# Performance work log

Hardware: AMD Instinct MI355X
Metric: run time of the kernel (lower is better)

The kernel has to match this reference:

```python
import jax, jax.numpy as jnp
import numpy as np

WSCALE = 0.05  # keep ReLU MLP activations in a sane range


def setup_inputs() -> dict:
    key = jax.random.key(0)
    ks = jax.random.split(key, 9)
    B, D, H = 2048, 64, 512
    return {
        "x": jax.random.normal(ks[0], (B, D), dtype=jnp.float32),
        "W1": jax.random.normal(ks[1], (H, D), dtype=jnp.float32) * WSCALE,
        "b1": jax.random.normal(ks[2], (H,), dtype=jnp.float32) * WSCALE,
        "W2": jax.random.normal(ks[3], (H, H), dtype=jnp.float32) * WSCALE,
        "b2": jax.random.normal(ks[4], (H,), dtype=jnp.float32) * WSCALE,
        "W3": jax.random.normal(ks[5], (H, H), dtype=jnp.float32) * WSCALE,
        "b3": jax.random.normal(ks[6], (H,), dtype=jnp.float32) * WSCALE,
        "W4": jax.random.normal(ks[7], (D, H), dtype=jnp.float32) * WSCALE,
        "b4": jax.random.normal(ks[8], (D,), dtype=jnp.float32) * WSCALE,
    }


def reference(x, W1, b1, W2, b2, W3, b3, W4, b4):
    # Score network: ReLU MLP (weights stored PyTorch-style [out, in]).
    a1 = x @ W1.T + b1          # [B, H]
    h1 = jax.nn.relu(a1)
    a2 = h1 @ W2.T + b2
    h2 = jax.nn.relu(a2)
    a3 = h2 @ W3.T + b3
    h3 = jax.nn.relu(a3)
    s = h3 @ W4.T + b4          # [B, D] score

    # Divergence = trace of Jacobian ds/dx per sample.
    # Per-sample J = W4 @ diag(m3) @ W3 @ diag(m2) @ W2 @ diag(m1) @ W1,
    # with m_k = 1[a_k > 0] (ReLU derivative; 0 at 0 like torch autograd).
    m1 = (a1 > 0).astype(x.dtype)
    m2 = (a2 > 0).astype(x.dtype)
    m3 = (a3 > 0).astype(x.dtype)
    T = m1[:, :, None] * W1[None, :, :]                 # [B, H, D]
    T = m2[:, :, None] * jnp.einsum('ij,bjd->bid', W2, T)  # [B, H, D]
    T = m3[:, :, None] * jnp.einsum('ij,bjd->bid', W3, T)  # [B, H, D]
    div = jnp.einsum('dj,bjd->b', W4, T)                # trace of J, [B]

    # Hyvarinen score: 0.5 * ||s||^2 + div
    val = 0.5 * jnp.sum(s * s, axis=1) + div
    return val
```

## Files before the change

kernel.cpp:

```cpp
#include <hip/hip_runtime.h>
#include <stdint.h>


typedef __attribute__((ext_vector_type(8))) short short8;
typedef __attribute__((ext_vector_type(4))) float f32x4;

union U16x8 {
  uint4 u;
  short8 s;
};

__device__ __forceinline__ uint16_t f2bf(float f) {
  uint32_t u = __float_as_uint(f);
  uint32_t lsb = (u >> 16) & 1u;
  u += 0x7FFFu + lsb;
  return (uint16_t)(u >> 16);
}

__device__ __forceinline__ void lds_load16(const uint4* gsrc, uint4* ldst) {
  __builtin_amdgcn_global_load_lds(
      (const __attribute__((address_space(1))) void*)gsrc,
      (__attribute__((address_space(3))) void*)ldst, 16, 0, 0);
}

__global__ __launch_bounds__(256) void convert_kernel(
    const float* __restrict__ W1, const float* __restrict__ W2,
    const float* __restrict__ W3, const float* __restrict__ W4,
    uint16_t* __restrict__ A2swz, uint16_t* __restrict__ A3swz,
    uint16_t* __restrict__ B1swz, uint16_t* __restrict__ B4swz,
    float* __restrict__ W2Tf, float* __restrict__ W3Tf,
    float* __restrict__ W1Tf, float* __restrict__ W4Tf) {
  const int i = blockIdx.x * 256 + threadIdx.x;
  if (i < 262144) {
    const int e = i;
    const int f = e >> 3, j = e & 7;
    const int lane = f & 63, fk = f >> 6;
    const int kc = fk & 15, r16 = fk >> 4;
    const int l15 = lane & 15, quad = lane >> 4;
    const int row = r16 * 16 + l15, col = kc * 32 + quad * 8 + j;
    A2swz[e] = f2bf(W2[row * 512 + col]);
  } else if (i < 524288) {
    const int e = i - 262144;
    const int f = e >> 3, j = e & 7;
    const int lane = f & 63, fk = f >> 6;
    const int kc = fk & 15, r16 = fk >> 4;
    const int l15 = lane & 15, quad = lane >> 4;
    const int row = r16 * 16 + l15, col = kc * 32 + quad * 8 + j;
    A3swz[e] = f2bf(W3[col * 512 + row]);
  } else if (i < 557056) {
    const int e = i - 524288;
    const int f = e >> 3, j = e & 7;
    const int lane = f & 63, fk = f >> 6;
    const int kc = fk >> 2, jt = fk & 3;
    const int l15 = lane & 15, quad = lane >> 4;
    const int d = jt * 16 + l15, col = kc * 32 + quad * 8 + j;
    B1swz[e] = f2bf(W1[col * 64 + d]);
  } else if (i < 589824) {
    const int e = i - 557056;
    const int f = e >> 3, j = e & 7;
    const int lane = f & 63, fk = f >> 6;
    const int kc = fk >> 2, jt = fk & 3;
    const int l15 = lane & 15, quad = lane >> 4;
    const int d = jt * 16 + l15, col = kc * 32 + quad * 8 + j;
    B4swz[e] = f2bf(W4[d * 512 + col]);
  } else if (i < 851968) {
    const int e = i - 589824;
    const int k = e >> 9, jj = e & 511;
    W2Tf[e] = W2[jj * 512 + k];
  } else if (i < 1114112) {
    const int e = i - 851968;
    const int k = e >> 9, jj = e & 511;
    W3Tf[e] = W3[jj * 512 + k];
  } else if (i < 1146880) {
    const int e = i - 1114112;
    const int k = e >> 9, jj = e & 511;
    W1Tf[e] = W1[jj * 64 + k];
  } else if (i < 1179648) {
    const int e = i - 1146880;
    const int k = e >> 6, d = e & 63;
    W4Tf[e] = W4[d * 512 + k];
  }
}

__device__ __forceinline__ void relu_store_mask4(
    float acc[4], float (*hdst)[4], uint32_t* __restrict__ mbase,
    int t, int lane, int wv) {
#pragma unroll
  for (int s = 0; s < 4; ++s) {
    const unsigned long long bal = __ballot(acc[s] > 0.f);
    if (lane == 0) {
      uint2 w2;
      w2.x = (uint32_t)bal;
      w2.y = (uint32_t)(bal >> 32);
      *(uint2*)(mbase + (size_t)s * 16 + 2 * wv) = w2;
    }
  }
  float4 r;
  r.x = acc[0] > 0.f ? acc[0] : 0.f;
  r.y = acc[1] > 0.f ? acc[1] : 0.f;
  r.z = acc[2] > 0.f ? acc[2] : 0.f;
  r.w = acc[3] > 0.f ? acc[3] : 0.f;
  *(float4*)&hdst[t][0] = r;
}

__global__ __launch_bounds__(512) void forward_kernel(
    const float* __restrict__ x,
    const float* __restrict__ W1Tf, const float* __restrict__ b1,
    const float* __restrict__ W2Tf, const float* __restrict__ b2,
    const float* __restrict__ W3Tf, const float* __restrict__ b3,
    const float* __restrict__ W4Tf, const float* __restrict__ b4,
    uint32_t* __restrict__ m1p, uint32_t* __restrict__ m2p,
    uint32_t* __restrict__ m3p, float* __restrict__ out) {
  __shared__ float xs[64][4];
  __shared__ float hA[512][4];
  __shared__ float hB[512][4];
  const int t = threadIdx.x;
  const int lane = t & 63, wv = t >> 6;
  const int b0 = blockIdx.x * 4;

  if (t < 256) {
    const int k = t >> 2, s = t & 3;
    xs[k][s] = x[(size_t)(b0 + s) * 64 + k];
  }
  __syncthreads();

  float acc[4];

  {
    const float bj = b1[t];
#pragma unroll
    for (int s = 0; s < 4; ++s) acc[s] = bj;
#pragma unroll 8
    for (int k = 0; k < 64; ++k) {
      const float w = W1Tf[(size_t)k * 512 + t];
      const float4 h = *(const float4*)&xs[k][0];
      acc[0] = fmaf(w, h.x, acc[0]); acc[1] = fmaf(w, h.y, acc[1]);
      acc[2] = fmaf(w, h.z, acc[2]); acc[3] = fmaf(w, h.w, acc[3]);
    }
    relu_store_mask4(acc, hA, m1p + (size_t)b0 * 16, t, lane, wv);
  }
  __syncthreads();

  {
    const float bj = b2[t];
#pragma unroll
    for (int s = 0; s < 4; ++s) acc[s] = bj;
#pragma unroll 8
    for (int k = 0; k < 512; ++k) {
      const float w = W2Tf[(size_t)k * 512 + t];
      const float4 h = *(const float4*)&hA[k][0];
      acc[0] = fmaf(w, h.x, acc[0]); acc[1] = fmaf(w, h.y, acc[1]);
      acc[2] = fmaf(w, h.z, acc[2]); acc[3] = fmaf(w, h.w, acc[3]);
    }
    relu_store_mask4(acc, hB, m2p + (size_t)b0 * 16, t, lane, wv);
  }
  __syncthreads();

  {
    const float bj = b3[t];
#pragma unroll
    for (int s = 0; s < 4; ++s) acc[s] = bj;
#pragma unroll 8
    for (int k = 0; k < 512; ++k) {
      const float w = W3Tf[(size_t)k * 512 + t];
      const float4 h = *(const float4*)&hB[k][0];
      acc[0] = fmaf(w, h.x, acc[0]); acc[1] = fmaf(w, h.y, acc[1]);
      acc[2] = fmaf(w, h.z, acc[2]); acc[3] = fmaf(w, h.w, acc[3]);
    }
    relu_store_mask4(acc, hA, m3p + (size_t)b0 * 16, t, lane, wv);
  }
  __syncthreads();

  if (wv < 4) {
    const int s = wv, d = lane;
    float a4 = b4[d];
#pragma unroll 8
    for (int k = 0; k < 512; ++k)
      a4 = fmaf(W4Tf[(size_t)k * 64 + d], hA[k][s], a4);
    float sq = a4 * a4;
#pragma unroll
    for (int off = 32; off; off >>= 1) sq += __shfl_down(sq, off, 64);
    if (lane == 0) out[b0 + s] = 0.5f * sq;
  }
}

__device__ __forceinline__ void expand_mask(uint32_t byte8, uint32_t mk[4]) {
#pragma unroll
  for (int i = 0; i < 4; ++i) {
    mk[i] = (((byte8 >> (2 * i)) & 1u) ? 0x0000FFFFu : 0u) |
            (((byte8 >> (2 * i + 1)) & 1u) ? 0xFFFF0000u : 0u);
  }
}

__global__ __launch_bounds__(256, 2) void div_kernel(
    const uint4* __restrict__ A2swz, const uint4* __restrict__ A3swz,
    const uint4* __restrict__ B1swz, const uint4* __restrict__ B4swz,
    const uint32_t* __restrict__ m1p, const uint32_t* __restrict__ m2p,
    const uint32_t* __restrict__ m3p, float* __restrict__ out) {
  __shared__ uint4 sfrag[3][16][64];
  __shared__ uint32_t smask[4][2][16];
  const int t = threadIdx.x;
  const int lane = t & 63, wv = t >> 6;
  const int quad = lane >> 4;
  const int g4 = blockIdx.x;
  const int rowB0 = blockIdx.y * 64;
  const int b = g4 * 4 + wv;
  const int r16b = blockIdx.y * 4;

  const uint4* sb = (wv == 0) ? A2swz : (wv == 1) ? A3swz : (wv == 2) ? B1swz : B4swz;

  f32x4 accC[4][4], accG[4][4];
#pragma unroll
  for (int it = 0; it < 4; ++it)
#pragma unroll
    for (int jt = 0; jt < 4; ++jt) {
      accC[it][jt] = (f32x4){0.f, 0.f, 0.f, 0.f};
      accG[it][jt] = (f32x4){0.f, 0.f, 0.f, 0.f};
    }

  {
    const uint32_t* m1w = m1p + (size_t)b * 16;
    const uint32_t* m3w = m3p + (size_t)b * 16;
    if (lane < 16) smask[wv][0][lane] = m1w[lane];
    else if (lane < 32) smask[wv][1][lane & 15] = m3w[lane & 15];
  }

  auto stage = [&](int sbuf, int kc) {
#pragma unroll
    for (int q = 0; q < 4; ++q) {
      const size_t off = (wv < 2)
          ? ((size_t)((r16b + q) * 16 + kc) * 64 + lane)
          : ((size_t)(kc * 4 + q) * 64 + lane);
      lds_load16(sb + off, &sfrag[sbuf][wv * 4 + q][0]);
    }
  };

  stage(0, 0);
  stage(1, 1);
  __builtin_amdgcn_sched_barrier(0);
  asm volatile("s_waitcnt vmcnt(4)" ::: "memory");
  __builtin_amdgcn_s_barrier();
  __builtin_amdgcn_sched_barrier(0);

#pragma unroll 1
  for (int kc = 0; kc < 16; ++kc) {
    const int rb = kc % 3;
    if (kc < 14) stage((kc + 2) % 3, kc + 2);

    const uint32_t m1d = __builtin_amdgcn_readfirstlane(smask[wv][0][kc]);
    const uint32_t m3d = __builtin_amdgcn_readfirstlane(smask[wv][1][kc]);

    uint4 a2[4], a3[4], u1[4], u4[4];
#pragma unroll
    for (int q = 0; q < 4; ++q) {
      a2[q] = sfrag[rb][q][lane];
      a3[q] = sfrag[rb][4 + q][lane];
      u1[q] = sfrag[rb][8 + q][lane];
      u4[q] = sfrag[rb][12 + q][lane];
    }

    uint32_t mk1[4], mk3[4];
    expand_mask((m1d >> (quad * 8)) & 0xFFu, mk1);
    expand_mask((m3d >> (quad * 8)) & 0xFFu, mk3);

    short8 bC[4];
#pragma unroll
    for (int jt = 0; jt < 4; ++jt) {
      U16x8 u;
      u.u = u1[jt];
      u.u.x &= mk1[0]; u.u.y &= mk1[1]; u.u.z &= mk1[2]; u.u.w &= mk1[3];
      bC[jt] = u.s;
    }
#pragma unroll
    for (int it = 0; it < 4; ++it) {
      U16x8 ua;
      ua.u = a2[it];
      const short8 af = ua.s;
#pragma unroll
      for (int jt = 0; jt < 4; ++jt)
        accC[it][jt] = __builtin_amdgcn_mfma_f32_16x16x32_bf16(af, bC[jt], accC[it][jt], 0, 0, 0);
    }
    short8 bG[4];
#pragma unroll
    for (int jt = 0; jt < 4; ++jt) {
      U16x8 u;
      u.u = u4[jt];
      u.u.x &= mk3[0]; u.u.y &= mk3[1]; u.u.z &= mk3[2]; u.u.w &= mk3[3];
      bG[jt] = u.s;
    }
#pragma unroll
    for (int it = 0; it < 4; ++it) {
      U16x8 ua;
      ua.u = a3[it];
      const short8 af = ua.s;
#pragma unroll
      for (int jt = 0; jt < 4; ++jt)
        accG[it][jt] = __builtin_amdgcn_mfma_f32_16x16x32_bf16(af, bG[jt], accG[it][jt], 0, 0, 0);
    }

    if (kc < 14) {
      asm volatile("s_waitcnt vmcnt(4)" ::: "memory");
    } else if (kc == 14) {
      asm volatile("s_waitcnt vmcnt(0)" ::: "memory");
    }
    if (kc < 15) {
      __builtin_amdgcn_s_barrier();
      __builtin_amdgcn_sched_barrier(0);
    }
  }

  const uint32_t* m2w = m2p + (size_t)b * 16;
  float dsum = 0.f;
#pragma unroll
  for (int it = 0; it < 4; ++it) {
    const int rloc = it * 16 + quad * 4;
    const uint32_t md = m2w[(rowB0 + rloc) >> 5];
    const uint32_t bits = (md >> (rloc & 31)) & 0xFu;
    const float w0 = (bits & 1u) ? 1.f : 0.f;
    const float w1 = (bits & 2u) ? 1.f : 0.f;
    const float w2 = (bits & 4u) ? 1.f : 0.f;
    const float w3 = (bits & 8u) ? 1.f : 0.f;
#pragma unroll
    for (int jt = 0; jt < 4; ++jt) {
      dsum = fmaf(w0, accC[it][jt][0] * accG[it][jt][0], dsum);
      dsum = fmaf(w1, accC[it][jt][1] * accG[it][jt][1], dsum);
      dsum = fmaf(w2, accC[it][jt][2] * accG[it][jt][2], dsum);
      dsum = fmaf(w3, accC[it][jt][3] * accG[it][jt][3], dsum);
    }
  }
#pragma unroll
  for (int off = 32; off; off >>= 1) dsum += __shfl_down(dsum, off, 64);
  if (lane == 0) atomicAdd(out + b, dsum);
}

extern "C" void kernel_launch(void* const* d_in, const int* in_sizes, int n_in,
                              void* d_out, int out_size, void* d_ws, size_t ws_size,
                              hipStream_t stream) {
  const float* x  = (const float*)d_in[0];
  const float* W1 = (const float*)d_in[1];
  const float* b1 = (const float*)d_in[2];
  const float* W2 = (const float*)d_in[3];
  const float* b2 = (const float*)d_in[4];
  const float* W3 = (const float*)d_in[5];
  const float* b3 = (const float*)d_in[6];
  const float* W4 = (const float*)d_in[7];
  const float* b4 = (const float*)d_in[8];
  float* out = (float*)d_out;

  char* ws = (char*)d_ws;
  uint16_t* A2swz = (uint16_t*)(ws + 0);
  uint16_t* A3swz = (uint16_t*)(ws + 524288);
  uint16_t* B1swz = (uint16_t*)(ws + 1048576);
  uint16_t* B4swz = (uint16_t*)(ws + 1114112);
  float*    W2Tf  = (float*)(ws + 1179648);
  float*    W3Tf  = (float*)(ws + 2228224);
  float*    W1Tf  = (float*)(ws + 3276800);
  float*    W4Tf  = (float*)(ws + 3407872);
  uint32_t* m1p   = (uint32_t*)(ws + 3538944);
  uint32_t* m2p   = (uint32_t*)(ws + 3670016);
  uint32_t* m3p   = (uint32_t*)(ws + 3801088);
  if (ws_size < 3932160) return;

  convert_kernel<<<4608, 256, 0, stream>>>(W1, W2, W3, W4,
                                           A2swz, A3swz, B1swz, B4swz,
                                           W2Tf, W3Tf, W1Tf, W4Tf);
  forward_kernel<<<512, 512, 0, stream>>>(x, W1Tf, b1, W2Tf, b2, W3Tf, b3,
                                          W4Tf, b4, m1p, m2p, m3p, out);
  div_kernel<<<dim3(512, 8), 256, 0, stream>>>((const uint4*)A2swz,
                                               (const uint4*)A3swz,
                                               (const uint4*)B1swz,
                                               (const uint4*)B4swz,
                                               m1p, m2p, m3p, out);
}
```

Before: 281.3 us.

## Software-pipeline forward weight loads, split output layer, and prioritize MFMA in divergence

The forward MLP layers now prefetch weight columns into double-buffered registers, eight rows ahead, so global loads overlap the FMA chain instead of stalling each iteration. The final W4 layer is split across all eight waves, with two K-halves per sample, four partial accumulators and an LDS reduction, instead of four waves doing the full serial K loop. In the divergence kernel, the two masked MFMA groups are split into separate scopes that each load only their own LDS fragments, and each MFMA burst is wrapped in s_setprio to favour matrix issue. The cost is more live registers and an extra barrier and LDS buffer in the forward kernel.

```diff
diff --git a/kernel.cpp b/kernel.cpp
--- a/kernel.cpp
+++ b/kernel.cpp
@@ -103,6 +103,45 @@
   *(float4*)&hdst[t][0] = r;
 }
 
+__device__ __forceinline__ void fwd_layer(
+    const float* __restrict__ WT, const float* __restrict__ bias,
+    const float (* __restrict__ src)[4], float (* __restrict__ dst)[4],
+    uint32_t* __restrict__ mbase, int t, int lane, int wv, int K) {
+  float acc[4];
+  {
+    const float bj = bias[t];
+    acc[0] = bj; acc[1] = bj; acc[2] = bj; acc[3] = bj;
+  }
+  const float* Wp = WT + t;
+  float wA[8], wB[8];
+#pragma unroll
+  for (int j = 0; j < 8; ++j) wA[j] = Wp[(size_t)j * 512];
+#pragma unroll 1
+  for (int kb = 0; kb < K; kb += 16) {
+#pragma unroll
+    for (int j = 0; j < 8; ++j) wB[j] = Wp[(size_t)(kb + 8 + j) * 512];
+#pragma unroll
+    for (int j = 0; j < 8; ++j) {
+      const float4 h = *(const float4*)&src[kb + j][0];
+      const float w = wA[j];
+      acc[0] = fmaf(w, h.x, acc[0]); acc[1] = fmaf(w, h.y, acc[1]);
+      acc[2] = fmaf(w, h.z, acc[2]); acc[3] = fmaf(w, h.w, acc[3]);
+    }
+    if (kb + 16 < K) {
+#pragma unroll
+      for (int j = 0; j < 8; ++j) wA[j] = Wp[(size_t)(kb + 16 + j) * 512];
+    }
+#pragma unroll
+    for (int j = 0; j < 8; ++j) {
+      const float4 h = *(const float4*)&src[kb + 8 + j][0];
+      const float w = wB[j];
+      acc[0] = fmaf(w, h.x, acc[0]); acc[1] = fmaf(w, h.y, acc[1]);
+      acc[2] = fmaf(w, h.z, acc[2]); acc[3] = fmaf(w, h.w, acc[3]);
+    }
+  }
+  relu_store_mask4(acc, dst, mbase, t, lane, wv);
+}
+
 __global__ __launch_bounds__(512) void forward_kernel(
     const float* __restrict__ x,
     const float* __restrict__ W1Tf, const float* __restrict__ b1,
@@ -114,6 +153,7 @@
   __shared__ float xs[64][4];
   __shared__ float hA[512][4];
   __shared__ float hB[512][4];
+  __shared__ float p4[4][2][64];
   const int t = threadIdx.x;
   const int lane = t & 63, wv = t >> 6;
   const int b0 = blockIdx.x * 4;
@@ -124,59 +164,42 @@
   }
   __syncthreads();
 
-  float acc[4];
+  fwd_layer(W1Tf, b1, xs, hA, m1p + (size_t)b0 * 16, t, lane, wv, 64);
+  __syncthreads();
+  fwd_layer(W2Tf, b2, hA, hB, m2p + (size_t)b0 * 16, t, lane, wv, 512);
+  __syncthreads();
+  fwd_layer(W3Tf, b3, hB, hA, m3p + (size_t)b0 * 16, t, lane, wv, 512);
+  __syncthreads();
 
   {
-    const float bj = b1[t];
-#pragma unroll
-    for (int s = 0; s < 4; ++s) acc[s] = bj;
-#pragma unroll 8
-    for (int k = 0; k < 64; ++k) {
-      const float w = W1Tf[(size_t)k * 512 + t];
-      const float4 h = *(const float4*)&xs[k][0];
-      acc[0] = fmaf(w, h.x, acc[0]); acc[1] = fmaf(w, h.y, acc[1]);
-      acc[2] = fmaf(w, h.z, acc[2]); acc[3] = fmaf(w, h.w, acc[3]);
-    }
-    relu_store_mask4(acc, hA, m1p + (size_t)b0 * 16, t, lane, wv);
+    const int s = wv & 3, hh = wv >> 2, d = lane;
+    const int k0 = hh * 256;
+    const float* Wp = W4Tf + (size_t)k0 * 64 + d;
+    float ap[4] = {0.f, 0.f, 0.f, 0.f};
+    float wA[8], wB[8];
+#pragma unroll
+    for (int j = 0; j < 8; ++j) wA[j] = Wp[(size_t)j * 64];
+#pragma unroll 1
+    for (int kb = 0; kb < 256; kb += 16) {
+#pragma unroll
+      for (int j = 0; j < 8; ++j) wB[j] = Wp[(size_t)(kb + 8 + j) * 64];
+#pragma unroll
+      for (int j = 0; j < 8; ++j)
+        ap[j & 3] = fmaf(wA[j], hA[k0 + kb + j][s], ap[j & 3]);
+      if (kb + 16 < 256) {
+#pragma unroll
+        for (int j = 0; j < 8; ++j) wA[j] = Wp[(size_t)(kb + 16 + j) * 64];
+      }
+#pragma unroll
+      for (int j = 0; j < 8; ++j)
+        ap[j & 3] = fmaf(wB[j], hA[k0 + kb + 8 + j][s], ap[j & 3]);
+    }
+    p4[s][hh][d] = (ap[0] + ap[1]) + (ap[2] + ap[3]);
   }
   __syncthreads();
-
-  {
-    const float bj = b2[t];
-#pragma unroll
-    for (int s = 0; s < 4; ++s) acc[s] = bj;
-#pragma unroll 8
-    for (int k = 0; k < 512; ++k) {
-      const float w = W2Tf[(size_t)k * 512 + t];
-      const float4 h = *(const float4*)&hA[k][0];
-      acc[0] = fmaf(w, h.x, acc[0]); acc[1] = fmaf(w, h.y, acc[1]);
-      acc[2] = fmaf(w, h.z, acc[2]); acc[3] = fmaf(w, h.w, acc[3]);
-    }
-    relu_store_mask4(acc, hB, m2p + (size_t)b0 * 16, t, lane, wv);
-  }
-  __syncthreads();
-
-  {
-    const float bj = b3[t];
-#pragma unroll
-    for (int s = 0; s < 4; ++s) acc[s] = bj;
-#pragma unroll 8
-    for (int k = 0; k < 512; ++k) {
-      const float w = W3Tf[(size_t)k * 512 + t];
-      const float4 h = *(const float4*)&hB[k][0];
-      acc[0] = fmaf(w, h.x, acc[0]); acc[1] = fmaf(w, h.y, acc[1]);
-      acc[2] = fmaf(w, h.z, acc[2]); acc[3] = fmaf(w, h.w, acc[3]);
-    }
-    relu_store_mask4(acc, hA, m3p + (size_t)b0 * 16, t, lane, wv);
-  }
-  __syncthreads();
-
   if (wv < 4) {
     const int s = wv, d = lane;
-    float a4 = b4[d];
-#pragma unroll 8
-    for (int k = 0; k < 512; ++k)
-      a4 = fmaf(W4Tf[(size_t)k * 64 + d], hA[k][s], a4);
+    const float a4 = p4[s][0][d] + p4[s][1][d] + b4[d];
     float sq = a4 * a4;
 #pragma unroll
     for (int off = 32; off; off >>= 1) sq += __shfl_down(sq, off, 64);
@@ -247,55 +270,68 @@
     const int rb = kc % 3;
     if (kc < 14) stage((kc + 2) % 3, kc + 2);
 
-    const uint32_t m1d = __builtin_amdgcn_readfirstlane(smask[wv][0][kc]);
-    const uint32_t m3d = __builtin_amdgcn_readfirstlane(smask[wv][1][kc]);
-
-    uint4 a2[4], a3[4], u1[4], u4[4];
-#pragma unroll
-    for (int q = 0; q < 4; ++q) {
-      a2[q] = sfrag[rb][q][lane];
-      a3[q] = sfrag[rb][4 + q][lane];
-      u1[q] = sfrag[rb][8 + q][lane];
-      u4[q] = sfrag[rb][12 + q][lane];
-    }
-
-    uint32_t mk1[4], mk3[4];
-    expand_mask((m1d >> (quad * 8)) & 0xFFu, mk1);
-    expand_mask((m3d >> (quad * 8)) & 0xFFu, mk3);
-
-    short8 bC[4];
-#pragma unroll
-    for (int jt = 0; jt < 4; ++jt) {
-      U16x8 u;
-      u.u = u1[jt];
-      u.u.x &= mk1[0]; u.u.y &= mk1[1]; u.u.z &= mk1[2]; u.u.w &= mk1[3];
-      bC[jt] = u.s;
-    }
-#pragma unroll
-    for (int it = 0; it < 4; ++it) {
-      U16x8 ua;
-      ua.u = a2[it];
-      const short8 af = ua.s;
-#pragma unroll
-      for (int jt = 0; jt < 4; ++jt)
-        accC[it][jt] = __builtin_amdgcn_mfma_f32_16x16x32_bf16(af, bC[jt], accC[it][jt], 0, 0, 0);
-    }
-    short8 bG[4];
-#pragma unroll
-    for (int jt = 0; jt < 4; ++jt) {
-      U16x8 u;
-      u.u = u4[jt];
-      u.u.x &= mk3[0]; u.u.y &= mk3[1]; u.u.z &= mk3[2]; u.u.w &= mk3[3];
-      bG[jt] = u.s;
-    }
-#pragma unroll
-    for (int it = 0; it < 4; ++it) {
-      U16x8 ua;
-      ua.u = a3[it];
-      const short8 af = ua.s;
-#pragma unroll
-      for (int jt = 0; jt < 4; ++jt)
-        accG[it][jt] = __builtin_amdgcn_mfma_f32_16x16x32_bf16(af, bG[jt], accG[it][jt], 0, 0, 0);
+    {
+      const uint32_t m1d = __builtin_amdgcn_readfirstlane(smask[wv][0][kc]);
+      uint32_t mk1[4];
+      expand_mask((m1d >> (quad * 8)) & 0xFFu, mk1);
+
+      uint4 a2[4], u1[4];
+#pragma unroll
+      for (int q = 0; q < 4; ++q) {
+        a2[q] = sfrag[rb][q][lane];
+        u1[q] = sfrag[rb][8 + q][lane];
+      }
+      short8 bC[4];
+#pragma unroll
+      for (int jt = 0; jt < 4; ++jt) {
+        U16x8 u;
+        u.u = u1[jt];
+        u.u.x &= mk1[0]; u.u.y &= mk1[1]; u.u.z &= mk1[2]; u.u.w &= mk1[3];
+        bC[jt] = u.s;
+      }
+      __builtin_amdgcn_s_setprio(1);
+#pragma unroll
+      for (int it = 0; it < 4; ++it) {
+        U16x8 ua;
+        ua.u = a2[it];
+        const short8 af = ua.s;
+#pragma unroll
+        for (int jt = 0; jt < 4; ++jt)
+          accC[it][jt] = __builtin_amdgcn_mfma_f32_16x16x32_bf16(af, bC[jt], accC[it][jt], 0, 0, 0);
+      }
+      __builtin_amdgcn_s_setprio(0);
+    }
+
+    {
+      const uint32_t m3d = __builtin_amdgcn_readfirstlane(smask[wv][1][kc]);
+      uint32_t mk3[4];
+      expand_mask((m3d >> (quad * 8)) & 0xFFu, mk3);
+
+      uint4 a3[4], u4[4];
+#pragma unroll
+      for (int q = 0; q < 4; ++q) {
+        a3[q] = sfrag[rb][4 + q][lane];
+        u4[q] = sfrag[rb][12 + q][lane];
+      }
+      short8 bG[4];
+#pragma unroll
+      for (int jt = 0; jt < 4; ++jt) {
+        U16x8 u;
+        u.u = u4[jt];
+        u.u.x &= mk3[0]; u.u.y &= mk3[1]; u.u.z &= mk3[2]; u.u.w &= mk3[3];
+        bG[jt] = u.s;
+      }
+      __builtin_amdgcn_s_setprio(1);
+#pragma unroll
+      for (int it = 0; it < 4; ++it) {
+        U16x8 ua;
+        ua.u = a3[it];
+        const short8 af = ua.s;
+#pragma unroll
+        for (int jt = 0; jt < 4; ++jt)
+          accG[it][jt] = __builtin_amdgcn_mfma_f32_16x16x32_bf16(af, bG[jt], accG[it][jt], 0, 0, 0);
+      }
+      __builtin_amdgcn_s_setprio(0);
     }
 
     if (kc < 14) {
```

New measurement: 280.0 us. No clear change (-0.4%).
